# Performance work log

Hardware: AMD Instinct MI355X
Metric: run time of the kernel (lower is better)

The kernel has to match this reference:

```python
import jax, jax.numpy as jnp
import numpy as np

B, S, H, L = 4096, 64, 768, 5
TEMP = 0.07
BN_EPS = 1e-5


def setup_inputs() -> dict:
    key = jax.random.key(0)
    ks = jax.random.split(key, 8)
    seq = jax.random.normal(ks[0], (B, S, H), dtype=jnp.float32)
    labels = jax.random.randint(ks[1], (B,), 0, L)
    s = 1.0 / np.sqrt(H)
    return {
        'sequence_output': seq,
        'cls_gamma': jnp.ones((H,), jnp.float32),
        'cls_beta': jnp.zeros((H,), jnp.float32),
        'cls_W': jax.random.normal(ks[2], (H, H), jnp.float32) * s,
        'cls_b': jax.random.normal(ks[3], (H,), jnp.float32) * 0.01,
        'label_gamma': jnp.ones((H,), jnp.float32),
        'label_beta': jnp.zeros((H,), jnp.float32),
        'label_W': jax.random.normal(ks[4], (H, H), jnp.float32) * s,
        'label_b': jax.random.normal(ks[5], (H,), jnp.float32) * 0.01,
        'labels': labels,
    }


def _batchnorm(x, gamma, beta):
    # training-mode BatchNorm1d: biased batch stats
    m = x.mean(0)
    v = jnp.mean((x - m) ** 2, axis=0)
    return (x - m) * jax.lax.rsqrt(v + BN_EPS) * gamma + beta


def _l2norm(x):
    return x / jnp.sqrt(jnp.sum(x * x, axis=-1, keepdims=True)).clip(1e-12)


def reference(sequence_output, cls_gamma, cls_beta, cls_W, cls_b,
              label_gamma, label_beta, label_W, label_b, labels):
    z = sequence_output[:, 0, :]  # [B,H]; dropout is identity in eval
    # label token spans: 'No relation' -> positions 1:3 (mean), rest single tokens 3..6
    theta = jnp.stack([
        sequence_output[:, 1:3, :].mean(axis=1),
        sequence_output[:, 3, :],
        sequence_output[:, 4, :],
        sequence_output[:, 5, :],
        sequence_output[:, 6, :],
    ], axis=1)  # [B,L,H]
    z_cl, theta_cl = z, theta

    zp = _batchnorm(z, cls_gamma, cls_beta) @ cls_W.T + cls_b  # [B,H]
    tp = _batchnorm(theta.reshape(-1, H), label_gamma, label_beta) @ label_W.T + label_b
    tp = tp.reshape(-1, L, H)  # [B,L,H]
    logits = jnp.einsum('blh,bh->bl', tp, zp)  # [B,L]

    # ---- dual supervised contrastive loss (vectorized over the python loops) ----
    z_norm = _l2norm(z_cl)        # [B,H]
    theta_norm = _l2norm(theta_cl)  # [B,L,H]
    same = labels[:, None] == labels[None, :]          # [B,B]
    eye = jnp.eye(labels.shape[0], dtype=bool)
    pos_mask = (same & ~eye).astype(jnp.float32)       # positives (same label, j != i)
    neg_mask = (~same).astype(jnp.float32)             # negatives (different label)
    has_pos = (same & ~eye).any(axis=1)

    # l_z: anchor z_i vs theta_j[labels_i] (pos) and all theta_j[:] for diff-label j (neg)
    expS = jnp.exp(jnp.einsum('ih,jlh->ijl', z_norm, theta_norm) / TEMP)  # [B,B,L]
    expS_at_lab = jnp.take_along_axis(
        expS, jnp.broadcast_to(labels[:, None, None], expS.shape[:2] + (1,)), axis=2
    )[..., 0]  # expS[i,j,labels[i]] -> [B,B]
    pos_z = jnp.sum(expS_at_lab * pos_mask, axis=1)
    neg_z = jnp.sum(expS.sum(axis=-1) * neg_mask, axis=1)
    l_z = jnp.where(has_pos, -jnp.log(pos_z / (pos_z + neg_z + 1e-8)), 0.0).sum()

    # l_theta: anchor theta_i[labels_i] vs z_j
    anchor_theta = jnp.take_along_axis(theta_norm, labels[:, None, None], axis=1)[:, 0, :]  # [B,H]
    expT = jnp.exp(anchor_theta @ z_norm.T / TEMP)  # [B,B]
    pos_t = jnp.sum(expT * pos_mask, axis=1)
    neg_t = jnp.sum(expT * neg_mask, axis=1)
    l_t = jnp.where(has_pos, -jnp.log(pos_t / (pos_t + neg_t + 1e-8)), 0.0).sum()

    dual_loss = (l_z + l_t) / labels.shape[0]
    return logits, dual_loss
```

## Files before the change

kernel.cpp:

```cpp
#include <hip/hip_runtime.h>
#include <hip/hip_bf16.h>
#include <cstdint>
#include <cstddef>

#define B_N 4096
#define S_N 64
#define H_N 768
#define L_N 5
#define TEMP_INV (1.0f / 0.07f)
#define BN_EPS 1e-5f

typedef __attribute__((ext_vector_type(8))) short short8;
typedef __attribute__((ext_vector_type(4))) float f32x4;

__device__ __forceinline__ void async_copy16(void* lds, const void* g) {
  __builtin_amdgcn_global_load_lds(
      (const __attribute__((address_space(1))) unsigned int*)g,
      (__attribute__((address_space(3))) unsigned int*)lds, 16, 0, 0);
}

__device__ __forceinline__ unsigned short bf16b(float x) {
  __hip_bfloat16 h = __float2bfloat16(x);
  return *reinterpret_cast<unsigned short*>(&h);
}
__device__ __forceinline__ void store_bf16x4(void* p, float4 v) {
  ushort4 o = make_ushort4(bf16b(v.x), bf16b(v.y), bf16b(v.z), bf16b(v.w));
  *reinterpret_cast<ushort4*>(p) = o;
}

__device__ inline float block_reduce_sum256(float v, float* sbuf) {
#pragma unroll
  for (int off = 32; off > 0; off >>= 1) v += __shfl_down(v, off, 64);
  int lane = threadIdx.x & 63;
  int wid = threadIdx.x >> 6;
  __syncthreads();
  if (lane == 0) sbuf[wid] = v;
  __syncthreads();
  float r = 0.f;
  if (threadIdx.x == 0) r = sbuf[0] + sbuf[1] + sbuf[2] + sbuf[3];
  return r;
}

__global__ __launch_bounds__(256) void extract_kernel(
    const float* __restrict__ seq, __hip_bfloat16* __restrict__ zb,
    __hip_bfloat16* __restrict__ tb, float* __restrict__ zn_inv,
    float* __restrict__ thn_inv, float* __restrict__ sum_z,
    float* __restrict__ ssq_z, float* __restrict__ sum_t,
    float* __restrict__ ssq_t) {
  __shared__ float pr[16][6][3];
  int t = threadIdx.x;
  int wv = t >> 6, ln = t & 63;
  bool act = t < 192;
  int c4 = t * 4;
  int b0 = blockIdx.x * 16;
  float zs[4] = {}, zq[4] = {}, ts4[4] = {}, tq4[4] = {};
  for (int r = 0; r < 16; ++r) {
    int b = b0 + r;
    const float* base = seq + (size_t)b * (S_N * H_N);
    float pv[6] = {0.f, 0.f, 0.f, 0.f, 0.f, 0.f};
    if (act) {
      float4 z4 = *(const float4*)(base + c4);
      store_bf16x4(zb + (size_t)b * H_N + c4, z4);
      pv[0] = z4.x * z4.x + z4.y * z4.y + z4.z * z4.z + z4.w * z4.w;
      zs[0] += z4.x; zs[1] += z4.y; zs[2] += z4.z; zs[3] += z4.w;
      zq[0] += z4.x * z4.x; zq[1] += z4.y * z4.y;
      zq[2] += z4.z * z4.z; zq[3] += z4.w * z4.w;
#pragma unroll
      for (int l = 0; l < L_N; ++l) {
        float4 v4;
        if (l == 0) {
          float4 a4 = *(const float4*)(base + H_N + c4);
          float4 b4 = *(const float4*)(base + 2 * H_N + c4);
          v4 = make_float4(0.5f * (a4.x + b4.x), 0.5f * (a4.y + b4.y),
                           0.5f * (a4.z + b4.z), 0.5f * (a4.w + b4.w));
        } else {
          v4 = *(const float4*)(base + (size_t)(l + 2) * H_N + c4);
        }
        store_bf16x4(tb + ((size_t)b * L_N + l) * H_N + c4, v4);
        pv[1 + l] = v4.x * v4.x + v4.y * v4.y + v4.z * v4.z + v4.w * v4.w;
        ts4[0] += v4.x; ts4[1] += v4.y; ts4[2] += v4.z; ts4[3] += v4.w;
        tq4[0] += v4.x * v4.x; tq4[1] += v4.y * v4.y;
        tq4[2] += v4.z * v4.z; tq4[3] += v4.w * v4.w;
      }
    }
#pragma unroll
    for (int v = 0; v < 6; ++v) {
      float x = pv[v];
#pragma unroll
      for (int off = 32; off > 0; off >>= 1) x += __shfl_down(x, off, 64);
      if (ln == 0 && wv < 3) pr[r][v][wv] = x;
    }
  }
  __syncthreads();
  if (t < 96) {
    int r = t / 6, v = t - r * 6;
    float s = pr[r][v][0] + pr[r][v][1] + pr[r][v][2];
    float inv = 1.f / fmaxf(sqrtf(s), 1e-12f);
    int b = b0 + r;
    if (v == 0) zn_inv[b] = inv;
    else thn_inv[b * L_N + (v - 1)] = inv;
  }
  if (act) {
#pragma unroll
    for (int j = 0; j < 4; ++j) {
      atomicAdd(&sum_z[c4 + j], zs[j]);
      atomicAdd(&ssq_z[c4 + j], zq[j]);
      atomicAdd(&sum_t[c4 + j], ts4[j]);
      atomicAdd(&ssq_t[c4 + j], tq4[j]);
    }
  }
}

__global__ void count_kernel(const int* __restrict__ labels, int* __restrict__ cnt) {
  int i = blockIdx.x * 256 + threadIdx.x;
  if (i < B_N) atomicAdd(&cnt[labels[i]], 1);
}

__global__ void finalize_kernel(
    const float* __restrict__ sum_z, const float* __restrict__ ssq_z,
    const float* __restrict__ sum_t, const float* __restrict__ ssq_t,
    const float* __restrict__ g_z, const float* __restrict__ b_z,
    const float* __restrict__ g_t, const float* __restrict__ b_t,
    float* __restrict__ sz_s, float* __restrict__ sz_t,
    float* __restrict__ st_s, float* __restrict__ st_t) {
  int h = blockIdx.x * 256 + threadIdx.x;
  if (h >= H_N) return;
  {
    float m = sum_z[h] * (1.f / B_N);
    float v = ssq_z[h] * (1.f / B_N) - m * m;
    float s = g_z[h] * rsqrtf(v + BN_EPS);
    sz_s[h] = s;
    sz_t[h] = b_z[h] - m * s;
  }
  {
    float m = sum_t[h] * (1.f / (B_N * L_N));
    float v = ssq_t[h] * (1.f / (B_N * L_N)) - m * m;
    float s = g_t[h] * rsqrtf(v + BN_EPS);
    st_s[h] = s;
    st_t[h] = b_t[h] - m * s;
  }
}

__global__ __launch_bounds__(256) void prep_cls_kernel(
    const float* __restrict__ W, const float* __restrict__ szs,
    const float* __restrict__ szt, const float* __restrict__ bias,
    __hip_bfloat16* __restrict__ Wb, float* __restrict__ cprime) {
  __shared__ float sbuf[4];
  int n = blockIdx.x;
  int t = threadIdx.x;
  float dot = 0.f;
  if (t < 192) {
    int c4 = t * 4;
    const float* row = W + (size_t)n * H_N;
    float4 w4 = *(const float4*)(row + c4);
    float4 s4 = *(const float4*)(szs + c4);
    float4 t4 = *(const float4*)(szt + c4);
    store_bf16x4(Wb + (size_t)n * H_N + c4,
                 make_float4(w4.x * s4.x, w4.y * s4.y, w4.z * s4.z, w4.w * s4.w));
    dot = w4.x * t4.x + w4.y * t4.y + w4.z * t4.z + w4.w * t4.w;
  }
  float s = block_reduce_sum256(dot, sbuf);
  if (t == 0) cprime[n] = s + bias[n];
}

__global__ __launch_bounds__(256) void transpose_wl_kernel(
    const float* __restrict__ Wl, __hip_bfloat16* __restrict__ WlT) {
  __shared__ float tile[32][33];
  int t = threadIdx.x;
  int tx = t & 31, ty0 = t >> 5;
  int n0 = blockIdx.x * 32, k0 = blockIdx.y * 32;
#pragma unroll
  for (int p = 0; p < 4; ++p)
    tile[ty0 + p * 8][tx] = Wl[(size_t)(n0 + ty0 + p * 8) * H_N + k0 + tx];
  __syncthreads();
#pragma unroll
  for (int p = 0; p < 4; ++p) {
    unsigned short us = bf16b(tile[tx][ty0 + p * 8]);
    *((unsigned short*)WlT + (size_t)(k0 + ty0 + p * 8) * H_N + n0 + tx) = us;
  }
}

template <bool WRITE_BF16, bool HAS_BIAS>
__global__ __launch_bounds__(256) void gemm128_kernel(
    const __hip_bfloat16* __restrict__ A, const __hip_bfloat16* __restrict__ Bm,
    const float* __restrict__ bias, float* __restrict__ outF,
    __hip_bfloat16* __restrict__ outB) {
  __shared__ __align__(16) __hip_bfloat16 Asm[128 * 32];
  __shared__ __align__(16) __hip_bfloat16 Bsm[128 * 32];
  int tid = threadIdx.x, lane = tid & 63, wid = tid >> 6;
  int wr = wid >> 1, wc = wid & 1;
  int i0 = blockIdx.x * 128, n0 = blockIdx.y * 128;
  int llo = lane & 15, lhi = lane >> 4;
  f32x4 acc[4][4] = {};
  for (int k0 = 0; k0 < H_N; k0 += 32) {
#pragma unroll
    for (int r = 0; r < 2; ++r) {
      int s = r * 256 + wid * 64 + lane;
      int row = s >> 2, kc = (s & 3) * 8;
      size_t go = (size_t)row * H_N + k0 + kc;
      async_copy16((char*)Asm + (size_t)(r * 256 + wid * 64) * 16,
                   A + (size_t)i0 * H_N + go);
      async_copy16((char*)Bsm + (size_t)(r * 256 + wid * 64) * 16,
                   Bm + (size_t)n0 * H_N + go);
    }
    __syncthreads();
    short8 a[4], b[4];
#pragma unroll
    for (int m = 0; m < 4; ++m)
      a[m] = *(const short8*)((const char*)Asm +
                              ((wr * 64 + m * 16 + llo) * 32 + lhi * 8) * 2);
#pragma unroll
    for (int n = 0; n < 4; ++n)
      b[n] = *(const short8*)((const char*)Bsm +
                              ((wc * 64 + n * 16 + llo) * 32 + lhi * 8) * 2);
#pragma unroll
    for (int m = 0; m < 4; ++m)
#pragma unroll
      for (int n = 0; n < 4; ++n)
        acc[m][n] =
            __builtin_amdgcn_mfma_f32_16x16x32_bf16(a[m], b[n], acc[m][n], 0, 0, 0);
    __syncthreads();
  }
#pragma unroll
  for (int n = 0; n < 4; ++n) {
    int col = n0 + wc * 64 + n * 16 + llo;
    float bv = HAS_BIAS ? bias[col] : 0.f;
#pragma unroll
    for (int m = 0; m < 4; ++m) {
#pragma unroll
      for (int r = 0; r < 4; ++r) {
        int row = i0 + wr * 64 + m * 16 + lhi * 4 + r;
        float val = acc[m][n][r] + bv;
        outF[(size_t)row * H_N + col] = val;
        if (WRITE_BF16)
          outB[(size_t)row * H_N + col] = __float2bfloat16(val);
      }
    }
  }
}

__global__ __launch_bounds__(256) void logits_kernel(
    const float* __restrict__ seq, const float* __restrict__ u,
    const float* __restrict__ zp, const float* __restrict__ st_s,
    const float* __restrict__ st_t, const float* __restrict__ label_b,
    float* __restrict__ out) {
  __shared__ float sbuf[4];
  int b = blockIdx.x;
  int t = threadIdx.x;
  bool act = t < 192;
  int c4 = t * 4;
  float4 w4 = make_float4(0.f, 0.f, 0.f, 0.f);
  float apart = 0.f;
  if (act) {
    float4 u4 = *(const float4*)(u + (size_t)b * H_N + c4);
    float4 zp4 = *(const float4*)(zp + (size_t)b * H_N + c4);
    float4 ss4 = *(const float4*)(st_s + c4);
    float4 tt4 = *(const float4*)(st_t + c4);
    float4 lb4 = *(const float4*)(label_b + c4);
    w4 = make_float4(u4.x * ss4.x, u4.y * ss4.y, u4.z * ss4.z, u4.w * ss4.w);
    apart = u4.x * tt4.x + u4.y * tt4.y + u4.z * tt4.z + u4.w * tt4.w +
            zp4.x * lb4.x + zp4.y * lb4.y + zp4.z * lb4.z + zp4.w * lb4.w;
  }
  float alpha = block_reduce_sum256(apart, sbuf);
  const float* base = seq + (size_t)b * (S_N * H_N);
#pragma unroll
  for (int l = 0; l < L_N; ++l) {
    float part = 0.f;
    if (act) {
      float4 v4;
      if (l == 0) {
        float4 a4 = *(const float4*)(base + H_N + c4);
        float4 b4 = *(const float4*)(base + 2 * H_N + c4);
        v4 = make_float4(0.5f * (a4.x + b4.x), 0.5f * (a4.y + b4.y),
                         0.5f * (a4.z + b4.z), 0.5f * (a4.w + b4.w));
      } else {
        v4 = *(const float4*)(base + (size_t)(l + 2) * H_N + c4);
      }
      part = v4.x * w4.x + v4.y * w4.y + v4.z * w4.z + v4.w * w4.w;
    }
    float s = block_reduce_sum256(part, sbuf);
    if (t == 0) out[b * L_N + l] = s + alpha;
  }
}

#define NT_K 12
__global__ __launch_bounds__(512, 1) void sgemm_fused_kernel(
    const __hip_bfloat16* __restrict__ zb, const __hip_bfloat16* __restrict__ tb,
    const float* __restrict__ zn_inv, const float* __restrict__ thn_inv,
    const int* __restrict__ labels, float* __restrict__ pos_z,
    float* __restrict__ neg_z, float* __restrict__ pos_t,
    float* __restrict__ neg_t) {
  __shared__ __align__(128) char ldsbuf[2][65536];

  const int tid = threadIdx.x;
  const int lane = tid & 63, wid = tid >> 6;
  const int llo = lane & 15, lhi = lane >> 4;
  const int wrbase = (wid >> 2) * 128;
  const int wcbase = (wid & 3) * 64;
  const int i0 = blockIdx.x * 256, n0 = blockIdx.y * 256;
  const int wvb = wid << 10;

  f32x4 acc[8][4] = {};

  auto stage = [&](int c, int kt) {
    char* dA = &ldsbuf[c][0];
    char* dB = &ldsbuf[c][32768];
#pragma unroll
    for (int w = 0; w < 4; ++w) {
      int s = w * 512 + tid;
      int row = s >> 3;
      int lq = (s & 7) ^ (row & 7);
      int kofs = kt * 64 + lq * 8;
      async_copy16(dA + w * 8192 + wvb, zb + (size_t)(i0 + row) * H_N + kofs);
      async_copy16(dB + w * 8192 + wvb, tb + (size_t)(n0 + row) * H_N + kofs);
    }
  };

  stage(0, 0);
  stage(1, 1);
  asm volatile("s_waitcnt vmcnt(8)" ::: "memory");
  __builtin_amdgcn_s_barrier();

  for (int t = 0; t < NT_K; ++t) {
    const char* ldsA = &ldsbuf[t & 1][0];
    const char* ldsB = &ldsbuf[t & 1][32768];
#pragma unroll
    for (int ks = 0; ks < 2; ++ks) {
      short8 a[8], b[4];
      int slot = ((ks * 4 + lhi) ^ (llo & 7)) * 16;
#pragma unroll
      for (int mi = 0; mi < 8; ++mi) {
        int row = wrbase + mi * 16 + llo;
        a[mi] = *(const short8*)(ldsA + row * 128 + slot);
      }
#pragma unroll
      for (int ni = 0; ni < 4; ++ni) {
        int col = wcbase + ni * 16 + llo;
        b[ni] = *(const short8*)(ldsB + col * 128 + slot);
      }
      __builtin_amdgcn_s_setprio(1);
#pragma unroll
      for (int mi = 0; mi < 8; ++mi)
#pragma unroll
        for (int ni = 0; ni < 4; ++ni)
          acc[mi][ni] = __builtin_amdgcn_mfma_f32_16x16x32_bf16(a[mi], b[ni],
                                                                acc[mi][ni], 0, 0, 0);
      __builtin_amdgcn_s_setprio(0);
    }
    asm volatile("s_waitcnt lgkmcnt(0)" ::: "memory");
    __builtin_amdgcn_s_barrier();
    if (t < NT_K - 2) {
      stage(t & 1, t + 2);
      asm volatile("s_waitcnt vmcnt(8)" ::: "memory");
    } else {
      asm volatile("s_waitcnt vmcnt(0)" ::: "memory");
    }
    __builtin_amdgcn_s_barrier();
  }
  __syncthreads();

  float* rpos = (float*)&ldsbuf[0][0];
  float* rneg = rpos + 256;
  float* cpos = rneg + 256;
  float* cneg = cpos + 256;
  float* rnorm = cneg + 256;
  float* cnorm = rnorm + 256;
  int* rowlab = (int*)(cnorm + 256);
  int* colj = rowlab + 256;
  int* coll = colj + 256;
  int* collab = coll + 256;

  if (tid < 256) {
    rowlab[tid] = labels[i0 + tid];
    rnorm[tid] = zn_inv[i0 + tid] * TEMP_INV;
    int c = n0 + tid;
    int j = c / 5;
    colj[tid] = j;
    coll[tid] = c - j * 5;
    collab[tid] = labels[j];
    cnorm[tid] = thn_inv[c];
    rpos[tid] = 0.f; rneg[tid] = 0.f; cpos[tid] = 0.f; cneg[tid] = 0.f;
  }
  __syncthreads();

  int cl[4], jg[4], lv[4], lj[4];
  float cs[4];
#pragma unroll
  for (int ni = 0; ni < 4; ++ni) {
    cl[ni] = wcbase + ni * 16 + llo;
    jg[ni] = colj[cl[ni]];
    lv[ni] = coll[cl[ni]];
    lj[ni] = collab[cl[ni]];
    cs[ni] = cnorm[cl[ni]];
  }
  float cpAcc[4] = {}, cnAcc[4] = {};
#pragma unroll
  for (int mi = 0; mi < 8; ++mi) {
#pragma unroll
    for (int r = 0; r < 4; ++r) {
      int rl = wrbase + mi * 16 + lhi * 4 + r;
      int ig = i0 + rl;
      int li = rowlab[rl];
      float rscale = rnorm[rl];
      float rp = 0.f, rn = 0.f;
#pragma unroll
      for (int ni = 0; ni < 4; ++ni) {
        float e = __expf(acc[mi][ni][r] * rscale * cs[ni]);
        bool same = (li == lj[ni]);
        bool diag = (ig == jg[ni]);
        if (same) {
          if (!diag && lv[ni] == li) { rp += e; cpAcc[ni] += e; }
        } else {
          rn += e;
          if (lv[ni] == lj[ni]) cnAcc[ni] += e;
        }
      }
      if (rp != 0.f) atomicAdd(&rpos[rl], rp);
      if (rn != 0.f) atomicAdd(&rneg[rl], rn);
    }
  }
#pragma unroll
  for (int ni = 0; ni < 4; ++ni) {
    if (cpAcc[ni] != 0.f) atomicAdd(&cpos[cl[ni]], cpAcc[ni]);
    if (cnAcc[ni] != 0.f) atomicAdd(&cneg[cl[ni]], cnAcc[ni]);
  }
  __syncthreads();
  if (tid < 256) {
    float v;
    v = rpos[tid]; if (v != 0.f) atomicAdd(&pos_z[i0 + tid], v);
    v = rneg[tid]; if (v != 0.f) atomicAdd(&neg_z[i0 + tid], v);
    int j = colj[tid];
    v = cpos[tid]; if (v != 0.f) atomicAdd(&pos_t[j], v);
    v = cneg[tid]; if (v != 0.f) atomicAdd(&neg_t[j], v);
  }
}

__global__ __launch_bounds__(256) void loss_kernel(
    const float* __restrict__ pos_z, const float* __restrict__ neg_z,
    const float* __restrict__ pos_t, const float* __restrict__ neg_t,
    const int* __restrict__ labels, const int* __restrict__ cnt,
    float* __restrict__ out_loss) {
  __shared__ float sbuf[4];
  int i = blockIdx.x * 256 + threadIdx.x;
  float term = 0.f;
  int li = labels[i];
  if (cnt[li] > 1) {
    float pz = pos_z[i], nz = neg_z[i];
    float pt = pos_t[i], nt = neg_t[i];
    term = -logf(pz / (pz + nz + 1e-8f)) - logf(pt / (pt + nt + 1e-8f));
  }
  float s = block_reduce_sum256(term, sbuf);
  if (threadIdx.x == 0) atomicAdd(out_loss, s * (1.0f / B_N));
}

extern "C" void kernel_launch(void* const* d_in, const int* in_sizes, int n_in,
                              void* d_out, int out_size, void* d_ws, size_t ws_size,
                              hipStream_t stream) {
  const float* seq = (const float*)d_in[0];
  const float* cls_gamma = (const float*)d_in[1];
  const float* cls_beta = (const float*)d_in[2];
  const float* cls_W = (const float*)d_in[3];
  const float* cls_b = (const float*)d_in[4];
  const float* label_gamma = (const float*)d_in[5];
  const float* label_beta = (const float*)d_in[6];
  const float* label_W = (const float*)d_in[7];
  const float* label_b = (const float*)d_in[8];
  const int* labels = (const int*)d_in[9];
  float* out = (float*)d_out;
  float* ws = (float*)d_ws;

  constexpr size_t OFF_SUMZ = 0;
  constexpr size_t OFF_SSQZ = 768;
  constexpr size_t OFF_SUMT = 1536;
  constexpr size_t OFF_SSQT = 2304;
  constexpr size_t OFF_POSZ = 3072;
  constexpr size_t OFF_NEGZ = 7168;
  constexpr size_t OFF_POST = 11264;
  constexpr size_t OFF_NEGT = 15360;
  constexpr size_t OFF_CNT = 19456;
  constexpr size_t ZERO_FLOATS = 19464;
  constexpr size_t OFF_SZS = 19464;
  constexpr size_t OFF_SZT = 20232;
  constexpr size_t OFF_STS = 21000;
  constexpr size_t OFF_STT = 21768;
  constexpr size_t OFF_ZNI = 22536;
  constexpr size_t OFF_TNI = 26632;
  constexpr size_t OFF_CPRIME = 47112;
  constexpr size_t OFF_ZP = 47880;
  constexpr size_t OFF_U = OFF_ZP + (size_t)B_N * H_N;
  constexpr size_t F32_END = OFF_U + (size_t)B_N * H_N;
  constexpr size_t BYTE_ZB = F32_END * sizeof(float);
  constexpr size_t BYTE_TB = BYTE_ZB + (size_t)B_N * H_N * 2;
  constexpr size_t BYTE_ZPB = BYTE_TB + (size_t)B_N * L_N * H_N * 2;
  constexpr size_t BYTE_WCB = BYTE_ZPB + (size_t)B_N * H_N * 2;
  constexpr size_t BYTE_WLT = BYTE_WCB + (size_t)H_N * H_N * 2;
  constexpr size_t TOTAL_BYTES = BYTE_WLT + (size_t)H_N * H_N * 2;
  if (ws_size < TOTAL_BYTES) return;

  __hip_bfloat16* zb = (__hip_bfloat16*)((char*)d_ws + BYTE_ZB);
  __hip_bfloat16* tb = (__hip_bfloat16*)((char*)d_ws + BYTE_TB);
  __hip_bfloat16* zpb = (__hip_bfloat16*)((char*)d_ws + BYTE_ZPB);
  __hip_bfloat16* wcb = (__hip_bfloat16*)((char*)d_ws + BYTE_WCB);
  __hip_bfloat16* wlt = (__hip_bfloat16*)((char*)d_ws + BYTE_WLT);

  hipMemsetAsync(d_ws, 0, ZERO_FLOATS * sizeof(float), stream);
  hipMemsetAsync((char*)d_out + (size_t)B_N * L_N * sizeof(float), 0, sizeof(float),
                 stream);

  extract_kernel<<<256, 256, 0, stream>>>(seq, zb, tb, ws + OFF_ZNI, ws + OFF_TNI,
                                          ws + OFF_SUMZ, ws + OFF_SSQZ,
                                          ws + OFF_SUMT, ws + OFF_SSQT);
  count_kernel<<<16, 256, 0, stream>>>(labels, (int*)(ws + OFF_CNT));
  finalize_kernel<<<3, 256, 0, stream>>>(
      ws + OFF_SUMZ, ws + OFF_SSQZ, ws + OFF_SUMT, ws + OFF_SSQT, cls_gamma,
      cls_beta, label_gamma, label_beta, ws + OFF_SZS, ws + OFF_SZT, ws + OFF_STS,
      ws + OFF_STT);
  prep_cls_kernel<<<H_N, 256, 0, stream>>>(cls_W, ws + OFF_SZS, ws + OFF_SZT, cls_b,
                                           wcb, ws + OFF_CPRIME);
  transpose_wl_kernel<<<dim3(24, 24), 256, 0, stream>>>(label_W, wlt);
  gemm128_kernel<true, true><<<dim3(32, 6), 256, 0, stream>>>(
      zb, wcb, ws + OFF_CPRIME, ws + OFF_ZP, zpb);
  gemm128_kernel<false, false><<<dim3(32, 6), 256, 0, stream>>>(
      zpb, wlt, nullptr, ws + OFF_U, nullptr);
  logits_kernel<<<B_N, 256, 0, stream>>>(seq, ws + OFF_U, ws + OFF_ZP, ws + OFF_STS,
                                         ws + OFF_STT, label_b, out);
  sgemm_fused_kernel<<<dim3(16, 80), 512, 0, stream>>>(
      zb, tb, ws + OFF_ZNI, ws + OFF_TNI, labels, ws + OFF_POSZ, ws + OFF_NEGZ,
      ws + OFF_POST, ws + OFF_NEGT);
  loss_kernel<<<16, 256, 0, stream>>>(ws + OFF_POSZ, ws + OFF_NEGZ, ws + OFF_POST,
                                      ws + OFF_NEGT, labels,
                                      (const int*)(ws + OFF_CNT),
                                      out + (size_t)B_N * L_N);
}
```

Before: 469.1 us.

## Interleave next-tile async loads with MFMA phases in similarity GEMM main loop

Restructures the K-loop of the fused similarity GEMM. The prefetch depth drops from two tiles ahead to one, and the global-to-LDS copy of the next tile is split into four parts, each issued during one of four MFMA sub-phases, with barriers between phases. The aim is to spread memory traffic across the compute and keep fewer fragment registers live, since only four A fragments are held at a time. In exchange it adds more barriers per iteration and a shorter prefetch distance, which could expose global load latency.

```diff
diff --git a/kernel.cpp b/kernel.cpp
--- a/kernel.cpp
+++ b/kernel.cpp
@@ -298,64 +298,58 @@
   const int wrbase = (wid >> 2) * 128;
   const int wcbase = (wid & 3) * 64;
   const int i0 = blockIdx.x * 256, n0 = blockIdx.y * 256;
-  const int wvb = wid << 10;
 
   f32x4 acc[8][4] = {};
 
-  auto stage = [&](int c, int kt) {
-    char* dA = &ldsbuf[c][0];
-    char* dB = &ldsbuf[c][32768];
-#pragma unroll
-    for (int w = 0; w < 4; ++w) {
-      int s = w * 512 + tid;
-      int row = s >> 3;
-      int lq = (s & 7) ^ (row & 7);
-      int kofs = kt * 64 + lq * 8;
-      async_copy16(dA + w * 8192 + wvb, zb + (size_t)(i0 + row) * H_N + kofs);
-      async_copy16(dB + w * 8192 + wvb, tb + (size_t)(n0 + row) * H_N + kofs);
-    }
+  auto stagePart = [&](int c, int kt, int p) {
+    int s = p * 512 + tid;
+    int row = s >> 3;
+    int lq = (s & 7) ^ (row & 7);
+    int kofs = kt * 64 + lq * 8;
+    int wub = (p * 512 + wid * 64) * 16;
+    async_copy16(&ldsbuf[c][0] + wub, zb + (size_t)(i0 + row) * H_N + kofs);
+    async_copy16(&ldsbuf[c][32768] + wub, tb + (size_t)(n0 + row) * H_N + kofs);
   };
 
-  stage(0, 0);
-  stage(1, 1);
-  asm volatile("s_waitcnt vmcnt(8)" ::: "memory");
+#pragma unroll
+  for (int p = 0; p < 4; ++p) stagePart(0, 0, p);
+  asm volatile("s_waitcnt vmcnt(0)" ::: "memory");
   __builtin_amdgcn_s_barrier();
 
   for (int t = 0; t < NT_K; ++t) {
     const char* ldsA = &ldsbuf[t & 1][0];
     const char* ldsB = &ldsbuf[t & 1][32768];
 #pragma unroll
-    for (int ks = 0; ks < 2; ++ks) {
-      short8 a[8], b[4];
-      int slot = ((ks * 4 + lhi) ^ (llo & 7)) * 16;
-#pragma unroll
-      for (int mi = 0; mi < 8; ++mi) {
-        int row = wrbase + mi * 16 + llo;
-        a[mi] = *(const short8*)(ldsA + row * 128 + slot);
+    for (int p = 0; p < 4; ++p) {
+      const int kk = p >> 1, mh = (p & 1) * 4;
+      const int slot = ((kk * 4 + lhi) ^ (llo & 7)) * 16;
+      short8 a[4], b[4];
+#pragma unroll
+      for (int m = 0; m < 4; ++m) {
+        int row = wrbase + (mh + m) * 16 + llo;
+        a[m] = *(const short8*)(ldsA + row * 128 + slot);
       }
 #pragma unroll
-      for (int ni = 0; ni < 4; ++ni) {
-        int col = wcbase + ni * 16 + llo;
-        b[ni] = *(const short8*)(ldsB + col * 128 + slot);
+      for (int n = 0; n < 4; ++n) {
+        int col = wcbase + n * 16 + llo;
+        b[n] = *(const short8*)(ldsB + col * 128 + slot);
       }
+      if (t + 1 < NT_K) stagePart((t + 1) & 1, t + 1, p);
+      __builtin_amdgcn_s_barrier();
+      asm volatile("s_waitcnt lgkmcnt(0)" ::: "memory");
+      __builtin_amdgcn_sched_barrier(0);
       __builtin_amdgcn_s_setprio(1);
 #pragma unroll
-      for (int mi = 0; mi < 8; ++mi)
-#pragma unroll
-        for (int ni = 0; ni < 4; ++ni)
-          acc[mi][ni] = __builtin_amdgcn_mfma_f32_16x16x32_bf16(a[mi], b[ni],
-                                                                acc[mi][ni], 0, 0, 0);
+      for (int m = 0; m < 4; ++m)
+#pragma unroll
+        for (int n = 0; n < 4; ++n)
+          acc[mh + m][n] = __builtin_amdgcn_mfma_f32_16x16x32_bf16(
+              a[m], b[n], acc[mh + m][n], 0, 0, 0);
       __builtin_amdgcn_s_setprio(0);
-    }
-    asm volatile("s_waitcnt lgkmcnt(0)" ::: "memory");
-    __builtin_amdgcn_s_barrier();
-    if (t < NT_K - 2) {
-      stage(t & 1, t + 2);
-      asm volatile("s_waitcnt vmcnt(8)" ::: "memory");
-    } else {
-      asm volatile("s_waitcnt vmcnt(0)" ::: "memory");
-    }
-    __builtin_amdgcn_s_barrier();
+      if (p == 3)
+        asm volatile("s_waitcnt vmcnt(0)" ::: "memory");
+      __builtin_amdgcn_s_barrier();
+    }
   }
   __syncthreads();
 
```

After: 455.9 us. 1.03x faster.
